# Kernel tuning notes

Hardware: AMD Instinct MI355X
Metric: run time of the kernel (lower is better)

## Reference

```python
import jax, jax.numpy as jnp
import numpy as np

B, M, N, D, H = 4, 8, 128, 32, 64
SMALL_V = 1e-8


def setup_inputs() -> dict:
    key = jax.random.key(0)
    ks = jax.random.split(key, 12)
    s = 0.05
    x = jax.random.normal(ks[0], (B, M, N, D), jnp.float32)
    sizes = jax.random.randint(ks[1], (B,), N // 2, N + 1)
    valid = (jnp.arange(N)[None, :] < sizes[:, None]).astype(jnp.float32)  # [B,N]
    x = x * valid[:, None, :, None]  # zero out padded items
    return {
        "x": x,
        "x_size": sizes.astype(jnp.float32),
        "W1a": jax.random.normal(ks[2], (D, 2 * D), jnp.float32) * s,
        "b1a": jax.random.normal(ks[3], (2 * D,), jnp.float32) * s,
        "W1b": jax.random.normal(ks[4], (2 * D, D), jnp.float32) * s,
        "b1b": jax.random.normal(ks[5], (D,), jnp.float32) * s,
        "W2a": jax.random.normal(ks[6], (D, 2 * D), jnp.float32) * s,
        "b2a": jax.random.normal(ks[7], (2 * D,), jnp.float32) * s,
        "W2b": jax.random.normal(ks[8], (2 * D, H), jnp.float32) * s,
        "b2b": jax.random.normal(ks[9], (H,), jnp.float32) * s,
        "w3": jax.random.normal(ks[10], (H,), jnp.float32) * s,
        "b3": jax.random.normal(ks[11], (1,), jnp.float32) * s,
    }


def _item_mask(x):
    # 1.0 where the item's feature row has any nonzero entry, else 0.0. [...,N,1]
    return jnp.any(x != 0, axis=-1, keepdims=True).astype(x.dtype)


def _set_norm(x, x_size):
    # layer_normalization with is_set_norm=True: normalize over (N*D) per set,
    # dividing by the true valid size x_size*D and masking padded items.
    b, m, n, d = x.shape
    mask = jnp.broadcast_to(_item_mask(x), x.shape).reshape(b, m, n * d)
    xr = x.reshape(b, m, n * d)
    denom = x_size[:, None] * d  # [B,1] -> broadcasts over nSet
    mean = jnp.sum(xr, axis=-1) / denom  # [B,M]
    diff = xr - mean[..., None]
    std = jnp.sqrt(jnp.sum(diff * diff * mask, axis=-1) / denom)  # [B,M]
    out = diff / (std[..., None] + SMALL_V) * mask
    return out.reshape(b, m, n, d)


def reference(x, x_size, W1a, b1a, W1b, b1b, W2a, b2a, W2b, b2b, w3, b3):
    mask = _item_mask(x)  # [B,M,N,1]
    x_orig = x
    xn = _set_norm(x, x_size) * mask  # [B,M,N,D]
    # MLP1 (rank-4 -> masked by its own input's item mask)
    m1 = _item_mask(xn)
    x1 = (jnp.matmul(jax.nn.gelu(jnp.matmul(xn, W1a) + b1a), W1b) + b1b) * m1
    # pairwise differences: x_diff[b,m,i,j,:] = x1[b,m,i,:] - xn[b,m,j,:]
    x_diff = x1[:, :, :, None, :] - xn[:, :, None, :, :]  # [B,M,N,N,D]
    # MLP2 (rank-5 -> no mask, is_SoftMax=0)
    e = jnp.matmul(jax.nn.gelu(jnp.matmul(x_diff, W2a) + b2a), W2b) + b2b  # [B,M,N,N,H]
    # aggregation: out[b,m,j,h,d] = sum_i e[b,m,i,j,h] * x1[b,m,i,d]
    agg = jnp.einsum('bmijh,bmid->bmjhd', e, x1)
    # MLP3_linear: Dense(1) over H, then squeeze
    out = jnp.einsum('bmjhd,h->bmjd', agg, w3) + b3[0]
    out = (out + x_orig) * mask
    return out
```

## Files before the change

kernel.cpp:

```cpp
#include <hip/hip_runtime.h>

#define BB 4
#define MM 8
#define BM 32
#define NN 128
#define DD 32
#define KK 64
constexpr int ND = NN * DD;
constexpr int NK = NN * KK;
#define SMALLV 1e-8f

__device__ __forceinline__ float gelu_t(float v) {
    float v2 = v * v;
    float u  = v * fmaf(0.044715f, v2, 1.0f) * 0.7978845608028654f;
    float e  = __builtin_amdgcn_exp2f(u * 2.8853900817779268f);
    float r  = __builtin_amdgcn_rcpf(e + 1.0f);
    float th = fmaf(-2.0f, r, 1.0f);
    float hv = 0.5f * v;
    return fmaf(hv, th, hv);
}

__global__ __launch_bounds__(512) void stats_kernel(
    const float* __restrict__ x, const float* __restrict__ x_size,
    float* __restrict__ statsg, float* __restrict__ maskg)
{
    __shared__ float sAny[NN];
    __shared__ float sRed[8];
    const int t = threadIdx.x, bm = blockIdx.x;
    const float* xp = x + (size_t)bm * ND;
    float v[8];
    float lsum = 0.f;
    #pragma unroll
    for (int s = 0; s < 8; ++s) { v[s] = xp[t + s * 512]; lsum += v[s]; }
    if (t < NN) sAny[t] = 0.f;
    __syncthreads();
    #pragma unroll
    for (int s = 0; s < 8; ++s) if (v[s] != 0.f) sAny[(t + s * 512) >> 5] = 1.f;
    #pragma unroll
    for (int off = 32; off; off >>= 1) lsum += __shfl_xor(lsum, off);
    if ((t & 63) == 0) sRed[t >> 6] = lsum;
    __syncthreads();
    float tot = 0.f;
    #pragma unroll
    for (int w = 0; w < 8; ++w) tot += sRed[w];
    const float denom = x_size[bm >> 3] * (float)DD;
    const float mean  = tot / denom;
    float lsq = 0.f;
    #pragma unroll
    for (int s = 0; s < 8; ++s) {
        float d = v[s] - mean;
        lsq += (sAny[(t + s * 512) >> 5] != 0.f) ? d * d : 0.f;
    }
    #pragma unroll
    for (int off = 32; off; off >>= 1) lsq += __shfl_xor(lsq, off);
    __syncthreads();
    if ((t & 63) == 0) sRed[t >> 6] = lsq;
    __syncthreads();
    float sq = 0.f;
    #pragma unroll
    for (int w = 0; w < 8; ++w) sq += sRed[w];
    const float inv = 1.f / (sqrtf(sq / denom) + SMALLV);
    if (t == 0) { statsg[bm * 2] = mean; statsg[bm * 2 + 1] = inv; }
    if (t < NN) maskg[bm * NN + t] = sAny[t];
}

__global__ __launch_bounds__(256) void mlp_kernel(
    const float* __restrict__ x, const float* __restrict__ statsg,
    const float* __restrict__ maskg,
    const float* __restrict__ W1a, const float* __restrict__ b1a,
    const float* __restrict__ W1b, const float* __restrict__ b1b,
    const float* __restrict__ W2a, const float* __restrict__ b2a,
    const float* __restrict__ W2b, const float* __restrict__ b2b,
    const float* __restrict__ w3,
    float* __restrict__ x1g, float* __restrict__ A1g, float* __restrict__ A2t,
    float* __restrict__ v2g, float* __restrict__ c3g)
{
    __shared__ float sXn[16 * DD];
    __shared__ float sH[16 * KK];
    __shared__ float sX1[16 * DD];
    const int t  = threadIdx.x;
    const int bm = blockIdx.x >> 3;
    const int nt = blockIdx.x & 7;
    const int n0 = nt * 16;
    const float mean = statsg[bm * 2], inv = statsg[bm * 2 + 1];

    #pragma unroll
    for (int s = 0; s < 2; ++s) {
        int idx = t + s * 256;
        float mk = maskg[bm * NN + n0 + (idx >> 5)];
        float xv = x[(size_t)bm * ND + n0 * DD + idx];
        sXn[idx] = (xv - mean) * inv * mk;
    }
    __syncthreads();

    const int k   = t & 63;
    const int ns0 = t >> 6;
    {
        float wc[DD];
        #pragma unroll
        for (int d = 0; d < DD; ++d) wc[d] = W1a[d * KK + k];
        float bk = b1a[k];
        #pragma unroll
        for (int r = 0; r < 4; ++r) {
            int n = ns0 + r * 4;
            const float* xr = &sXn[n * DD];
            float acc = bk;
            #pragma unroll
            for (int d = 0; d < DD; ++d) acc = fmaf(xr[d], wc[d], acc);
            sH[n * KK + k] = gelu_t(acc);
        }
    }
    __syncthreads();

    {
        const int d2  = t & 31;
        const int ns1 = t >> 5;
        float wc[KK];
        #pragma unroll
        for (int q = 0; q < KK; ++q) wc[q] = W1b[q * DD + d2];
        float bd = b1b[d2];
        #pragma unroll
        for (int r = 0; r < 2; ++r) {
            int n = ns1 + r * 8;
            const float* hr = &sH[n * KK];
            float acc = bd;
            #pragma unroll
            for (int q = 0; q < KK; ++q) acc = fmaf(hr[q], wc[q], acc);
            float val = acc * maskg[bm * NN + n0 + n];
            sX1[n * DD + d2] = val;
            x1g[(size_t)bm * ND + (n0 + n) * DD + d2] = val;
        }
    }
    __syncthreads();

    {
        float wc[DD];
        #pragma unroll
        for (int d = 0; d < DD; ++d) wc[d] = W2a[d * KK + k];
        float bk = b2a[k];
        #pragma unroll
        for (int r = 0; r < 4; ++r) {
            int n = ns0 + r * 4;
            const float* x1r = &sX1[n * DD];
            const float* xnr = &sXn[n * DD];
            float a1 = bk, a2 = 0.f;
            #pragma unroll
            for (int d = 0; d < DD; ++d) {
                a1 = fmaf(x1r[d], wc[d], a1);
                a2 = fmaf(xnr[d], wc[d], a2);
            }
            A1g[(size_t)bm * NK + (n0 + n) * KK + k] = a1;
            A2t[(size_t)bm * NK + k * NN + (n0 + n)] = a2;
        }
    }

    if (blockIdx.x == 0) {
        if (t < KK) {
            float acc = 0.f;
            for (int h = 0; h < KK; ++h) acc += W2b[t * KK + h] * w3[h];
            v2g[t] = acc;
        }
        if (t == 0) {
            float acc = 0.f;
            for (int h = 0; h < KK; ++h) acc += b2b[h] * w3[h];
            c3g[0] = acc;
        }
    }
}

__global__ __launch_bounds__(256) void pair_kernel(
    const float* __restrict__ A1g, const float* __restrict__ A2t,
    const float* __restrict__ x1g, const float* __restrict__ v2g,
    const float* __restrict__ c3g, float* __restrict__ partial)
{
    __shared__ float sA1[16 * KK];
    __shared__ float sX1[16 * DD];
    __shared__ float sV2[KK];
    __shared__ float sPart[4][64][DD + 1];
    const int t    = threadIdx.x;
    const int bm   = blockIdx.x >> 4;
    const int jg   = (blockIdx.x >> 3) & 1;
    const int ig   = blockIdx.x & 7;
    const int w    = t >> 6;
    const int lane = t & 63;

    #pragma unroll
    for (int s = 0; s < 4; ++s)
        sA1[t + s * 256] = A1g[(size_t)bm * NK + ig * 1024 + t + s * 256];
    #pragma unroll
    for (int s = 0; s < 2; ++s)
        sX1[t + s * 256] = x1g[(size_t)bm * ND + ig * 512 + t + s * 256];
    if (t < KK) sV2[t] = v2g[t];
    const float c3 = c3g[0];

    float a2r[KK];
    #pragma unroll
    for (int q = 0; q < KK; ++q)
        a2r[q] = A2t[(size_t)bm * NK + q * NN + jg * 64 + lane];

    float acc[DD];
    #pragma unroll
    for (int d = 0; d < DD; ++d) acc[d] = 0.f;
    __syncthreads();

    const float4* v2f = (const float4*)sV2;
    #pragma unroll
    for (int ii = 0; ii < 4; ++ii) {
        const int i = w * 4 + ii;
        const float4* a1f = (const float4*)&sA1[i * KK];
        const float4* x1f = (const float4*)&sX1[i * DD];
        float S = c3;
        #pragma unroll
        for (int kq = 0; kq < 16; ++kq) {
            float4 a  = a1f[kq];
            float4 vv = v2f[kq];
            S = fmaf(gelu_t(a.x - a2r[kq * 4 + 0]), vv.x, S);
            S = fmaf(gelu_t(a.y - a2r[kq * 4 + 1]), vv.y, S);
            S = fmaf(gelu_t(a.z - a2r[kq * 4 + 2]), vv.z, S);
            S = fmaf(gelu_t(a.w - a2r[kq * 4 + 3]), vv.w, S);
        }
        #pragma unroll
        for (int dq = 0; dq < 8; ++dq) {
            float4 xv = x1f[dq];
            acc[dq * 4 + 0] = fmaf(S, xv.x, acc[dq * 4 + 0]);
            acc[dq * 4 + 1] = fmaf(S, xv.y, acc[dq * 4 + 1]);
            acc[dq * 4 + 2] = fmaf(S, xv.z, acc[dq * 4 + 2]);
            acc[dq * 4 + 3] = fmaf(S, xv.w, acc[dq * 4 + 3]);
        }
    }
    #pragma unroll
    for (int d = 0; d < DD; ++d) sPart[w][lane][d] = acc[d];
    __syncthreads();

    const size_t base = (size_t)blockIdx.x * 2048;
    #pragma unroll
    for (int s = 0; s < 8; ++s) {
        int idx = t + s * 256;
        int jl = idx >> 5, d = idx & 31;
        partial[base + idx] =
            sPart[0][jl][d] + sPart[1][jl][d] + sPart[2][jl][d] + sPart[3][jl][d];
    }
}

__global__ __launch_bounds__(256) void final_kernel(
    const float* __restrict__ x, const float* __restrict__ b3,
    const float* __restrict__ partial, float* __restrict__ out)
{
    const int gid = blockIdx.x * 256 + threadIdx.x;
    const int j = gid >> 5;
    const int bm = j >> 7, jg = (j >> 6) & 1, jl = j & 63;
    const size_t pb = ((size_t)(bm * 2 + jg) * 8) * 2048 + (jl << 5) + (gid & 31);
    float sum = 0.f;
    #pragma unroll
    for (int ig = 0; ig < 8; ++ig) sum += partial[pb + ig * 2048];
    float xv = x[gid];
    unsigned long long bal = __ballot(xv != 0.f);
    int lane = threadIdx.x & 63;
    unsigned long long half = (lane < 32) ? (bal & 0xFFFFFFFFull) : (bal >> 32);
    float mk = half ? 1.f : 0.f;
    out[gid] = (sum + b3[0] + xv) * mk;
}

extern "C" void kernel_launch(void* const* d_in, const int* in_sizes, int n_in,
                              void* d_out, int out_size, void* d_ws, size_t ws_size,
                              hipStream_t stream) {
    const float* x      = (const float*)d_in[0];
    const float* x_size = (const float*)d_in[1];
    const float* W1a    = (const float*)d_in[2];
    const float* b1a    = (const float*)d_in[3];
    const float* W1b    = (const float*)d_in[4];
    const float* b1b    = (const float*)d_in[5];
    const float* W2a    = (const float*)d_in[6];
    const float* b2a    = (const float*)d_in[7];
    const float* W2b    = (const float*)d_in[8];
    const float* b2b    = (const float*)d_in[9];
    const float* w3     = (const float*)d_in[10];
    const float* b3     = (const float*)d_in[11];
    float* out = (float*)d_out;

    float* ws      = (float*)d_ws;
    float* statsg  = ws;
    float* maskg   = statsg + 64;
    float* x1g     = maskg + 4096;
    float* A1g     = x1g + (size_t)BM * ND;
    float* A2t     = A1g + (size_t)BM * NK;
    float* v2g     = A2t + (size_t)BM * NK;
    float* c3g     = v2g + KK;
    float* partial = c3g + 64;

    stats_kernel<<<BM, 512, 0, stream>>>(x, x_size, statsg, maskg);
    mlp_kernel<<<BM * 8, 256, 0, stream>>>(x, statsg, maskg,
        W1a, b1a, W1b, b1b, W2a, b2a, W2b, b2b, w3,
        x1g, A1g, A2t, v2g, c3g);
    pair_kernel<<<BM * 16, 256, 0, stream>>>(A1g, A2t, x1g, v2g, c3g, partial);
    final_kernel<<<512, 256, 0, stream>>>(x, b3, partial, out);
}
```

Measured before the change: 107.5 us.

## Halve per-block row tiles to double grid size and stage MLP weights in LDS

The MLP and pair kernels now handle 8 rows per block instead of 16, doubling their grid sizes (256 and 1024 blocks) so more of the GPU's compute units are occupied. The MLP kernel copies the W1a, W1b and W2a weights and their biases into shared memory once per block rather than loading weight columns into registers from global memory. The pair kernel interleaves two i rows per wavefront to expose more independent GELU work. The cost is twice as many partial-sum slabs for the final kernel to read and reduce, and more redundant weight loading across blocks.

```diff
diff --git a/kernel.cpp b/kernel.cpp
--- a/kernel.cpp
+++ b/kernel.cpp
@@ -75,83 +75,79 @@
     float* __restrict__ x1g, float* __restrict__ A1g, float* __restrict__ A2t,
     float* __restrict__ v2g, float* __restrict__ c3g)
 {
-    __shared__ float sXn[16 * DD];
-    __shared__ float sH[16 * KK];
-    __shared__ float sX1[16 * DD];
+    __shared__ float sW1a[DD * KK];
+    __shared__ float sW1b[KK * DD];
+    __shared__ float sW2a[DD * KK];
+    __shared__ float sXn[8 * DD];
+    __shared__ float sH[8 * KK];
+    __shared__ float sX1[8 * DD];
+    __shared__ float sB1a[KK], sB2a[KK], sB1b[DD];
+
     const int t  = threadIdx.x;
-    const int bm = blockIdx.x >> 3;
-    const int nt = blockIdx.x & 7;
-    const int n0 = nt * 16;
+    const int bm = blockIdx.x >> 4;
+    const int nt = blockIdx.x & 15;
+    const int n0 = nt * 8;
     const float mean = statsg[bm * 2], inv = statsg[bm * 2 + 1];
 
-    #pragma unroll
-    for (int s = 0; s < 2; ++s) {
-        int idx = t + s * 256;
-        float mk = maskg[bm * NN + n0 + (idx >> 5)];
-        float xv = x[(size_t)bm * ND + n0 * DD + idx];
-        sXn[idx] = (xv - mean) * inv * mk;
-    }
-    __syncthreads();
-
-    const int k   = t & 63;
-    const int ns0 = t >> 6;
-    {
-        float wc[DD];
-        #pragma unroll
-        for (int d = 0; d < DD; ++d) wc[d] = W1a[d * KK + k];
-        float bk = b1a[k];
-        #pragma unroll
-        for (int r = 0; r < 4; ++r) {
-            int n = ns0 + r * 4;
-            const float* xr = &sXn[n * DD];
-            float acc = bk;
-            #pragma unroll
-            for (int d = 0; d < DD; ++d) acc = fmaf(xr[d], wc[d], acc);
-            sH[n * KK + k] = gelu_t(acc);
-        }
-    }
-    __syncthreads();
-
-    {
-        const int d2  = t & 31;
-        const int ns1 = t >> 5;
-        float wc[KK];
-        #pragma unroll
-        for (int q = 0; q < KK; ++q) wc[q] = W1b[q * DD + d2];
-        float bd = b1b[d2];
-        #pragma unroll
-        for (int r = 0; r < 2; ++r) {
-            int n = ns1 + r * 8;
-            const float* hr = &sH[n * KK];
-            float acc = bd;
-            #pragma unroll
-            for (int q = 0; q < KK; ++q) acc = fmaf(hr[q], wc[q], acc);
-            float val = acc * maskg[bm * NN + n0 + n];
-            sX1[n * DD + d2] = val;
-            x1g[(size_t)bm * ND + (n0 + n) * DD + d2] = val;
-        }
-    }
-    __syncthreads();
-
-    {
-        float wc[DD];
-        #pragma unroll
-        for (int d = 0; d < DD; ++d) wc[d] = W2a[d * KK + k];
-        float bk = b2a[k];
-        #pragma unroll
-        for (int r = 0; r < 4; ++r) {
-            int n = ns0 + r * 4;
-            const float* x1r = &sX1[n * DD];
-            const float* xnr = &sXn[n * DD];
-            float a1 = bk, a2 = 0.f;
-            #pragma unroll
-            for (int d = 0; d < DD; ++d) {
-                a1 = fmaf(x1r[d], wc[d], a1);
-                a2 = fmaf(xnr[d], wc[d], a2);
-            }
-            A1g[(size_t)bm * NK + (n0 + n) * KK + k] = a1;
-            A2t[(size_t)bm * NK + k * NN + (n0 + n)] = a2;
-        }
+    {
+        const float4* a4 = (const float4*)W1a;
+        const float4* b4 = (const float4*)W1b;
+        const float4* c4 = (const float4*)W2a;
+        float4* sa = (float4*)sW1a; float4* sb = (float4*)sW1b; float4* sc = (float4*)sW2a;
+        sa[t] = a4[t]; sa[t + 256] = a4[t + 256];
+        sb[t] = b4[t]; sb[t + 256] = b4[t + 256];
+        sc[t] = c4[t]; sc[t + 256] = c4[t + 256];
+    }
+    if (t < KK) { sB1a[t] = b1a[t]; sB2a[t] = b2a[t]; }
+    if (t < DD) { sB1b[t] = b1b[t]; }
+
+    {
+        float mk = maskg[bm * NN + n0 + (t >> 5)];
+        float xv = x[(size_t)bm * ND + n0 * DD + t];
+        sXn[t] = (xv - mean) * inv * mk;
+    }
+    __syncthreads();
+
+    const int k    = t & 63;
+    const int slot = t >> 6;
+
+    #pragma unroll
+    for (int r = 0; r < 2; ++r) {
+        int n = slot + r * 4;
+        const float* xr = &sXn[n * DD];
+        float acc = sB1a[k];
+        #pragma unroll
+        for (int d = 0; d < DD; ++d) acc = fmaf(xr[d], sW1a[d * KK + k], acc);
+        sH[n * KK + k] = gelu_t(acc);
+    }
+    __syncthreads();
+
+    {
+        const int d2 = t & 31;
+        const int n  = t >> 5;
+        const float* hr = &sH[n * KK];
+        float acc = sB1b[d2];
+        #pragma unroll
+        for (int q = 0; q < KK; ++q) acc = fmaf(hr[q], sW1b[q * DD + d2], acc);
+        float val = acc * maskg[bm * NN + n0 + n];
+        sX1[n * DD + d2] = val;
+        x1g[(size_t)bm * ND + (n0 + n) * DD + d2] = val;
+    }
+    __syncthreads();
+
+    #pragma unroll
+    for (int r = 0; r < 2; ++r) {
+        int n = slot + r * 4;
+        const float* x1r = &sX1[n * DD];
+        const float* xnr = &sXn[n * DD];
+        float a1 = sB2a[k], a2 = 0.f;
+        #pragma unroll
+        for (int d = 0; d < DD; ++d) {
+            a1 = fmaf(x1r[d], sW2a[d * KK + k], a1);
+            a2 = fmaf(xnr[d], sW2a[d * KK + k], a2);
+        }
+        A1g[(size_t)bm * NK + (n0 + n) * KK + k] = a1;
+        A2t[(size_t)bm * NK + k * NN + (n0 + n)] = a2;
     }
 
     if (blockIdx.x == 0) {
@@ -173,23 +169,20 @@
     const float* __restrict__ x1g, const float* __restrict__ v2g,
     const float* __restrict__ c3g, float* __restrict__ partial)
 {
-    __shared__ float sA1[16 * KK];
-    __shared__ float sX1[16 * DD];
+    __shared__ float sA1[8 * KK];
+    __shared__ float sX1[8 * DD];
     __shared__ float sV2[KK];
     __shared__ float sPart[4][64][DD + 1];
     const int t    = threadIdx.x;
-    const int bm   = blockIdx.x >> 4;
-    const int jg   = (blockIdx.x >> 3) & 1;
-    const int ig   = blockIdx.x & 7;
+    const int bm   = blockIdx.x >> 5;
+    const int jg   = (blockIdx.x >> 4) & 1;
+    const int ig   = blockIdx.x & 15;
     const int w    = t >> 6;
     const int lane = t & 63;
 
-    #pragma unroll
-    for (int s = 0; s < 4; ++s)
-        sA1[t + s * 256] = A1g[(size_t)bm * NK + ig * 1024 + t + s * 256];
-    #pragma unroll
-    for (int s = 0; s < 2; ++s)
-        sX1[t + s * 256] = x1g[(size_t)bm * ND + ig * 512 + t + s * 256];
+    sA1[t]       = A1g[(size_t)bm * NK + ig * 512 + t];
+    sA1[t + 256] = A1g[(size_t)bm * NK + ig * 512 + t + 256];
+    sX1[t]       = x1g[(size_t)bm * ND + ig * 256 + t];
     if (t < KK) sV2[t] = v2g[t];
     const float c3 = c3g[0];
 
@@ -204,28 +197,35 @@
     __syncthreads();
 
     const float4* v2f = (const float4*)sV2;
-    #pragma unroll
-    for (int ii = 0; ii < 4; ++ii) {
-        const int i = w * 4 + ii;
-        const float4* a1f = (const float4*)&sA1[i * KK];
-        const float4* x1f = (const float4*)&sX1[i * DD];
-        float S = c3;
+    {
+        const int i0 = w * 2, i1 = w * 2 + 1;
+        const float4* a1f0 = (const float4*)&sA1[i0 * KK];
+        const float4* a1f1 = (const float4*)&sA1[i1 * KK];
+        const float4* x1f0 = (const float4*)&sX1[i0 * DD];
+        const float4* x1f1 = (const float4*)&sX1[i1 * DD];
+        float S0 = c3, S1 = c3;
         #pragma unroll
         for (int kq = 0; kq < 16; ++kq) {
-            float4 a  = a1f[kq];
+            float4 a0 = a1f0[kq];
+            float4 a1 = a1f1[kq];
             float4 vv = v2f[kq];
-            S = fmaf(gelu_t(a.x - a2r[kq * 4 + 0]), vv.x, S);
-            S = fmaf(gelu_t(a.y - a2r[kq * 4 + 1]), vv.y, S);
-            S = fmaf(gelu_t(a.z - a2r[kq * 4 + 2]), vv.z, S);
-            S = fmaf(gelu_t(a.w - a2r[kq * 4 + 3]), vv.w, S);
+            S0 = fmaf(gelu_t(a0.x - a2r[kq * 4 + 0]), vv.x, S0);
+            S1 = fmaf(gelu_t(a1.x - a2r[kq * 4 + 0]), vv.x, S1);
+            S0 = fmaf(gelu_t(a0.y - a2r[kq * 4 + 1]), vv.y, S0);
+            S1 = fmaf(gelu_t(a1.y - a2r[kq * 4 + 1]), vv.y, S1);
+            S0 = fmaf(gelu_t(a0.z - a2r[kq * 4 + 2]), vv.z, S0);
+            S1 = fmaf(gelu_t(a1.z - a2r[kq * 4 + 2]), vv.z, S1);
+            S0 = fmaf(gelu_t(a0.w - a2r[kq * 4 + 3]), vv.w, S0);
+            S1 = fmaf(gelu_t(a1.w - a2r[kq * 4 + 3]), vv.w, S1);
         }
         #pragma unroll
         for (int dq = 0; dq < 8; ++dq) {
-            float4 xv = x1f[dq];
-            acc[dq * 4 + 0] = fmaf(S, xv.x, acc[dq * 4 + 0]);
-            acc[dq * 4 + 1] = fmaf(S, xv.y, acc[dq * 4 + 1]);
-            acc[dq * 4 + 2] = fmaf(S, xv.z, acc[dq * 4 + 2]);
-            acc[dq * 4 + 3] = fmaf(S, xv.w, acc[dq * 4 + 3]);
+            float4 xa = x1f0[dq];
+            float4 xb = x1f1[dq];
+            acc[dq * 4 + 0] = fmaf(S0, xa.x, fmaf(S1, xb.x, acc[dq * 4 + 0]));
+            acc[dq * 4 + 1] = fmaf(S0, xa.y, fmaf(S1, xb.y, acc[dq * 4 + 1]));
+            acc[dq * 4 + 2] = fmaf(S0, xa.z, fmaf(S1, xb.z, acc[dq * 4 + 2]));
+            acc[dq * 4 + 3] = fmaf(S0, xa.w, fmaf(S1, xb.w, acc[dq * 4 + 3]));
         }
     }
     #pragma unroll
@@ -249,10 +249,10 @@
     const int gid = blockIdx.x * 256 + threadIdx.x;
     const int j = gid >> 5;
     const int bm = j >> 7, jg = (j >> 6) & 1, jl = j & 63;
-    const size_t pb = ((size_t)(bm * 2 + jg) * 8) * 2048 + (jl << 5) + (gid & 31);
+    const size_t pb = ((size_t)(bm * 2 + jg) * 16) * 2048 + (jl << 5) + (gid & 31);
     float sum = 0.f;
     #pragma unroll
-    for (int ig = 0; ig < 8; ++ig) sum += partial[pb + ig * 2048];
+    for (int ig = 0; ig < 16; ++ig) sum += partial[pb + ig * 2048];
     float xv = x[gid];
     unsigned long long bal = __ballot(xv != 0.f);
     int lane = threadIdx.x & 63;
@@ -289,9 +289,9 @@
     float* partial = c3g + 64;
 
     stats_kernel<<<BM, 512, 0, stream>>>(x, x_size, statsg, maskg);
-    mlp_kernel<<<BM * 8, 256, 0, stream>>>(x, statsg, maskg,
+    mlp_kernel<<<BM * 16, 256, 0, stream>>>(x, statsg, maskg,
         W1a, b1a, W1b, b1b, W2a, b2a, W2b, b2b, w3,
         x1g, A1g, A2t, v2g, c3g);
-    pair_kernel<<<BM * 16, 256, 0, stream>>>(A1g, A2t, x1g, v2g, c3g, partial);
+    pair_kernel<<<BM * 32, 256, 0, stream>>>(A1g, A2t, x1g, v2g, c3g, partial);
     final_kernel<<<512, 256, 0, stream>>>(x, b3, partial, out);
 }
```

Result: no change. 108.1 us (+0.5%).
